# Kernel optimization log

Hardware: AMD Instinct MI355X
Metric: run time of the kernel (lower is better)

## Reference

```python
import jax, jax.numpy as jnp
import numpy as np

LEVELS = np.array([8, 5, 5, 5], dtype=np.int64)
BASIS = np.cumprod(np.concatenate([[1], LEVELS[:-1]])).astype(np.int64)  # [1,8,40,200]
N_E = int(np.prod(LEVELS))  # 1000
BN_EPS = 1e-5
BOUND_EPS = 1e-3


def setup_inputs() -> dict:
    key = jax.random.key(0)
    ks = jax.random.split(key, 3)
    B, C, T, E = 32, 512, 4096, 4
    return {
        "z": jax.random.normal(ks[0], (B, C, T), dtype=jnp.float32),
        "W_in": jax.random.normal(ks[1], (C, E), dtype=jnp.float32) * 0.05,
        "b_in": jnp.zeros((E,), dtype=jnp.float32),
        "gamma": jnp.ones((E,), dtype=jnp.float32),
        "beta": jnp.zeros((E,), dtype=jnp.float32),
        "W_out": jax.random.normal(ks[2], (E, C), dtype=jnp.float32) * 0.05,
        "b_out": jnp.zeros((C,), dtype=jnp.float32),
    }


def _round_ste(x):
    return x + jax.lax.stop_gradient(jnp.round(x) - x)


def reference(z, W_in, b_in, gamma, beta, W_out, b_out):
    levels = jnp.asarray(LEVELS, dtype=jnp.float32)      # [E]
    basis = jnp.asarray(BASIS, dtype=jnp.float32)        # [E]
    half_w = jnp.floor(levels / 2.0)                     # levels // 2
    B, C, T = z.shape
    N = B * T

    # preprocess: 'n c t -> (n t) c'
    x = jnp.transpose(z, (0, 2, 1)).reshape(N, C)        # [N, C]
    # project_in
    h = x @ W_in + b_in                                   # [N, E]
    # BatchNorm1d, training mode (biased batch stats)
    mu = jnp.mean(h, axis=0)
    var = jnp.var(h, axis=0)
    h = (h - mu) * jax.lax.rsqrt(var + BN_EPS) * gamma + beta

    # bound + round_ste quantize
    half_l = (levels - 1.0) * (1.0 - BOUND_EPS) / 2.0
    offset = jnp.where(jnp.mod(levels, 2.0) == 0.0, 0.5, 0.0)
    shift = jnp.tan(offset / half_l)
    bounded = jnp.tanh(h + shift) * half_l - offset
    zhat_n = _round_ste(bounded) / half_w                 # [N, E], normalized codes

    # codes -> indices
    idx = jnp.sum((zhat_n * half_w + half_w) * basis, axis=-1).astype(jnp.int32)  # [N]

    # project_out, '(b t) c -> b c t'
    out = zhat_n @ W_out + b_out                          # [N, C]
    zhat = jnp.transpose(out.reshape(B, T, C), (0, 2, 1))  # [B, C, T]

    commit_loss = jnp.mean((z - jax.lax.stop_gradient(zhat)) ** 2)

    # perplexity via counts (avoids [N, n_e] one-hot)
    counts = jnp.zeros((N_E,), dtype=jnp.float32).at[idx].add(1.0)
    e_mean = counts / N
    perplexity = jnp.exp(-jnp.sum(e_mean * jnp.log(e_mean + 1e-10)))

    return zhat, commit_loss, perplexity
```

## Files before the change

### kernel.cpp

```cpp
#include <hip/hip_runtime.h>
#include <math.h>


namespace {
constexpr int Bv = 32, Cv = 512, Tv = 4096;
constexpr int Nv = Bv * Tv;
constexpr long long TOTv = (long long)Nv * Cv;
constexpr int NTILES = Nv / 256;
constexpr int CSPLIT = 4;
constexpr int CL = Cv / CSPLIT;

constexpr size_t OFF_H   = 0;
constexpr size_t OFF_G   = OFF_H  + (size_t)Nv * 4 * sizeof(double);
constexpr size_t OFF_BS  = OFF_G  + (size_t)Nv * 4 * sizeof(float);
constexpr size_t OFF_CST = OFF_BS + (size_t)NTILES * 10 * sizeof(double);
constexpr size_t OFF_CNT = OFF_CST + 32 * sizeof(double);
constexpr size_t OFF_CP  = OFF_CNT + 4096;
constexpr size_t OFF_WD  = OFF_CP  + (size_t)NTILES * sizeof(double);
constexpr size_t OFF_WT  = OFF_WD  + 2048 * sizeof(double);
}

__global__ void fsq_k0(const float* __restrict__ W_in, const float* __restrict__ W_out,
                       double* __restrict__ winD, float* __restrict__ woutT)
{
    const int i = blockIdx.x * 256 + threadIdx.x;
    if (i < 2048) {
        winD[i] = (double)W_in[i];
        const int c = i >> 2, e = i & 3;
        woutT[i] = W_out[e * 512 + c];
    }
}

__global__ __launch_bounds__(256) void fsq_kA(
    const float* __restrict__ z, const double* __restrict__ winD,
    const float* __restrict__ woutT, const float* __restrict__ b_out,
    const float* __restrict__ b_in,
    double* __restrict__ h_ws, float* __restrict__ g_ws, double* __restrict__ bs_ws)
{
    __shared__ double red[256][10];
    const int tid = threadIdx.x;
    const int blk = blockIdx.x;
    const int b = blk >> 4;
    const int tile = blk & 15;
    const int t = tile * 256 + tid;
    const float* zp = z + (size_t)b * Cv * Tv + t;

    double h0 = 0.0, h1 = 0.0, h2 = 0.0, h3 = 0.0;
    float g0 = 0.f, g1 = 0.f, g2 = 0.f, g3 = 0.f, zbp = 0.f, z2p = 0.f;
#pragma unroll 8
    for (int c = 0; c < Cv; ++c) {
        const float zv = zp[(size_t)c * Tv];
        const double zd = (double)zv;
        h0 = fma(zd, winD[c * 4 + 0], h0);
        h1 = fma(zd, winD[c * 4 + 1], h1);
        h2 = fma(zd, winD[c * 4 + 2], h2);
        h3 = fma(zd, winD[c * 4 + 3], h3);
        g0 = fmaf(zv, woutT[c * 4 + 0], g0);
        g1 = fmaf(zv, woutT[c * 4 + 1], g1);
        g2 = fmaf(zv, woutT[c * 4 + 2], g2);
        g3 = fmaf(zv, woutT[c * 4 + 3], g3);
        zbp = fmaf(zv, b_out[c], zbp);
        z2p = fmaf(zv, zv, z2p);
    }
    h0 += (double)b_in[0]; h1 += (double)b_in[1];
    h2 += (double)b_in[2]; h3 += (double)b_in[3];

    const int n = blk * 256 + tid;
    double* hp = h_ws + (size_t)n * 4;
    double2 hA; hA.x = h0; hA.y = h1;
    double2 hB; hB.x = h2; hB.y = h3;
    *(double2*)(hp)     = hA;
    *(double2*)(hp + 2) = hB;
    *(float4*)(g_ws + (size_t)n * 4) = make_float4(g0, g1, g2, g3);

    red[tid][0] = h0; red[tid][1] = h1; red[tid][2] = h2; red[tid][3] = h3;
    red[tid][4] = h0 * h0; red[tid][5] = h1 * h1; red[tid][6] = h2 * h2; red[tid][7] = h3 * h3;
    red[tid][8] = (double)z2p; red[tid][9] = (double)zbp;
    __syncthreads();
    for (int s = 128; s > 0; s >>= 1) {
        if (tid < s) {
#pragma unroll
            for (int k = 0; k < 10; ++k) red[tid][k] += red[tid + s][k];
        }
        __syncthreads();
    }
    if (tid == 0) {
#pragma unroll
        for (int k = 0; k < 10; ++k) bs_ws[blk * 10 + k] = red[0][k];
    }
}

__global__ __launch_bounds__(512) void fsq_kB(
    const float* __restrict__ gamma, const float* __restrict__ beta,
    const float* __restrict__ W_out, const float* __restrict__ b_out,
    const double* __restrict__ bs_ws, double* __restrict__ consts,
    unsigned* __restrict__ counts)
{
    __shared__ double buf[512 * 15];
    const int tid = threadIdx.x;
#pragma unroll
    for (int k = 0; k < 10; ++k) buf[tid * 15 + k] = bs_ws[tid * 10 + k];
    __syncthreads();
    for (int s = 256; s > 0; s >>= 1) {
        if (tid < s) {
#pragma unroll
            for (int k = 0; k < 10; ++k) buf[tid * 15 + k] += buf[(tid + s) * 15 + k];
        }
        __syncthreads();
    }
    double Sh[4] = {0, 0, 0, 0}, Sq[4] = {0, 0, 0, 0}, SZ2 = 0, SZB = 0;
    if (tid == 0) {
        Sh[0] = buf[0]; Sh[1] = buf[1]; Sh[2] = buf[2]; Sh[3] = buf[3];
        Sq[0] = buf[4]; Sq[1] = buf[5]; Sq[2] = buf[6]; Sq[3] = buf[7];
        SZ2 = buf[8]; SZB = buf[9];
    }
    __syncthreads();
    {
        const int c = tid;
        const double w0 = W_out[c], w1 = W_out[512 + c], w2 = W_out[1024 + c], w3 = W_out[1536 + c];
        const double bb = b_out[c];
        double* r = buf + tid * 15;
        r[0] = w0 * w0; r[1] = w0 * w1; r[2] = w0 * w2; r[3] = w0 * w3;
        r[4] = w1 * w1; r[5] = w1 * w2; r[6] = w1 * w3;
        r[7] = w2 * w2; r[8] = w2 * w3; r[9] = w3 * w3;
        r[10] = w0 * bb; r[11] = w1 * bb; r[12] = w2 * bb; r[13] = w3 * bb; r[14] = bb * bb;
    }
    __syncthreads();
    for (int s = 256; s > 0; s >>= 1) {
        if (tid < s) {
#pragma unroll
            for (int k = 0; k < 15; ++k) buf[tid * 15 + k] += buf[(tid + s) * 15 + k];
        }
        __syncthreads();
    }
    if (tid == 0) {
        const double Ninv = 1.0 / (double)Nv;
#pragma unroll
        for (int e = 0; e < 4; ++e) {
            const double mu = Sh[e] * Ninv;
            const double var = Sq[e] * Ninv - mu * mu;
            const double sc = (double)gamma[e] / sqrt(var + 1e-5);
            consts[e] = sc;
            consts[4 + e] = (double)beta[e] - mu * sc;
        }
        consts[8 + 0]  = buf[0]; consts[8 + 1]  = buf[1]; consts[8 + 2]  = buf[2]; consts[8 + 3]  = buf[3];
        consts[8 + 4]  = buf[1]; consts[8 + 5]  = buf[4]; consts[8 + 6]  = buf[5]; consts[8 + 7]  = buf[6];
        consts[8 + 8]  = buf[2]; consts[8 + 9]  = buf[5]; consts[8 + 10] = buf[7]; consts[8 + 11] = buf[8];
        consts[8 + 12] = buf[3]; consts[8 + 13] = buf[6]; consts[8 + 14] = buf[8]; consts[8 + 15] = buf[9];
        consts[24] = buf[10]; consts[25] = buf[11]; consts[26] = buf[12]; consts[27] = buf[13];
        consts[28] = buf[14];
        consts[29] = SZ2; consts[30] = SZB;
        consts[31] = tan(0.5 / ((8.0 - 1.0) * (1.0 - 1e-3) / 2.0));
    }
    for (int i = tid; i < 1000; i += 512) counts[i] = 0;
}

__global__ __launch_bounds__(256) void fsq_kC(
    const float* __restrict__ woutT, const float* __restrict__ b_out,
    const double* __restrict__ h_ws, const float* __restrict__ g_ws,
    const double* __restrict__ consts, unsigned* __restrict__ counts,
    double* __restrict__ cp_ws, float* __restrict__ out)
{
    __shared__ double red[256];
    const int tid = threadIdx.x;
    const int nt = blockIdx.x;
    const int ys = blockIdx.y;
    const int n = nt * 256 + tid;

    const double sc0 = consts[0], sc1 = consts[1], sc2 = consts[2], sc3 = consts[3];
    const double bi0 = consts[4], bi1 = consts[5], bi2 = consts[6], bi3 = consts[7];
    const double shift0 = consts[31];

    const double* hp = h_ws + (size_t)n * 4;
    const double hn0 = fma(hp[0], sc0, bi0);
    const double hn1 = fma(hp[1], sc1, bi1);
    const double hn2 = fma(hp[2], sc2, bi2);
    const double hn3 = fma(hp[3], sc3, bi3);

    constexpr double hl0 = (8.0 - 1.0) * (1.0 - 1e-3) / 2.0;
    constexpr double hl1 = (5.0 - 1.0) * (1.0 - 1e-3) / 2.0;
    const double r0 = rint(tanh(hn0 + shift0) * hl0 - 0.5);
    const double r1 = rint(tanh(hn1) * hl1);
    const double r2 = rint(tanh(hn2) * hl1);
    const double r3 = rint(tanh(hn3) * hl1);
    const double zd0 = r0 * 0.25, zd1 = r1 * 0.5, zd2 = r2 * 0.5, zd3 = r3 * 0.5;
    const float zn0 = (float)zd0, zn1 = (float)zd1, zn2 = (float)zd2, zn3 = (float)zd3;

    if (ys == 0) {
        const int code = ((int)r0 + 4) + ((int)r1 + 2) * 8 + ((int)r2 + 2) * 40 + ((int)r3 + 2) * 200;
        atomicAdd(&counts[code], 1u);
        const float4 gv = *(const float4*)(g_ws + (size_t)n * 4);
        const double cg = zd0 * (double)gv.x + zd1 * (double)gv.y
                        + zd2 * (double)gv.z + zd3 * (double)gv.w;
        const double znd[4] = {zd0, zd1, zd2, zd3};
        double q = consts[28] + 2.0 * (zd0 * consts[24] + zd1 * consts[25]
                                     + zd2 * consts[26] + zd3 * consts[27]);
#pragma unroll
        for (int e = 0; e < 4; ++e)
#pragma unroll
            for (int f = 0; f < 4; ++f)
                q = fma(znd[e] * znd[f], consts[8 + e * 4 + f], q);
        red[tid] = q - 2.0 * cg;
        __syncthreads();
        for (int s = 128; s > 0; s >>= 1) {
            if (tid < s) red[tid] += red[tid + s];
            __syncthreads();
        }
        if (tid == 0) cp_ws[nt] = red[0];
    }

    const int c0 = ys * CL;
    const size_t base = (size_t)(n >> 12) * ((size_t)Cv * Tv) + (size_t)(n & (Tv - 1));
#pragma unroll 8
    for (int i = 0; i < CL; ++i) {
        const int c = c0 + i;
        float val = b_out[c];
        val = fmaf(zn0, woutT[c * 4 + 0], val);
        val = fmaf(zn1, woutT[c * 4 + 1], val);
        val = fmaf(zn2, woutT[c * 4 + 2], val);
        val = fmaf(zn3, woutT[c * 4 + 3], val);
        out[base + (size_t)c * Tv] = val;
    }
}

__global__ __launch_bounds__(512) void fsq_kD(
    const double* __restrict__ cp_ws, const double* __restrict__ consts,
    const unsigned* __restrict__ counts, float* __restrict__ out, int out_size)
{
    __shared__ double rc[512];
    __shared__ double rp[512];
    const int tid = threadIdx.x;
    double c_ = cp_ws[tid];
    double p_ = 0.0;
    for (int i = tid; i < 1000; i += 512) {
        const double em = (double)counts[i] / (double)Nv;
        p_ += em * log(em + 1e-10);
    }
    rc[tid] = c_; rp[tid] = p_;
    __syncthreads();
    for (int s = 256; s > 0; s >>= 1) {
        if (tid < s) { rc[tid] += rc[tid + s]; rp[tid] += rp[tid + s]; }
        __syncthreads();
    }
    if (tid == 0) {
        const double commit = (consts[29] - 2.0 * consts[30] + rc[0]) / (double)TOTv;
        out[out_size - 2] = (float)commit;
        out[out_size - 1] = (float)exp(-rp[0]);
    }
}

extern "C" void kernel_launch(void* const* d_in, const int* in_sizes, int n_in,
                              void* d_out, int out_size, void* d_ws, size_t ws_size,
                              hipStream_t stream) {
    const float* z     = (const float*)d_in[0];
    const float* W_in  = (const float*)d_in[1];
    const float* b_in  = (const float*)d_in[2];
    const float* gamma = (const float*)d_in[3];
    const float* beta  = (const float*)d_in[4];
    const float* W_out = (const float*)d_in[5];
    const float* b_out = (const float*)d_in[6];
    float* out = (float*)d_out;

    char* ws = (char*)d_ws;
    double*   h_ws   = (double*)(ws + OFF_H);
    float*    g_ws   = (float*)(ws + OFF_G);
    double*   bs_ws  = (double*)(ws + OFF_BS);
    double*   consts = (double*)(ws + OFF_CST);
    unsigned* counts = (unsigned*)(ws + OFF_CNT);
    double*   cp_ws  = (double*)(ws + OFF_CP);
    double*   winD   = (double*)(ws + OFF_WD);
    float*    woutT  = (float*)(ws + OFF_WT);

    fsq_k0<<<8, 256, 0, stream>>>(W_in, W_out, winD, woutT);
    fsq_kA<<<NTILES, 256, 0, stream>>>(z, winD, woutT, b_out, b_in, h_ws, g_ws, bs_ws);
    fsq_kB<<<1, 512, 0, stream>>>(gamma, beta, W_out, b_out, bs_ws, consts, counts);
    fsq_kC<<<dim3(NTILES, CSPLIT), 256, 0, stream>>>(woutT, b_out, h_ws, g_ws, consts,
                                                     counts, cp_ws, out);
    fsq_kD<<<1, 512, 0, stream>>>(cp_ws, consts, counts, out, out_size);
}
```

Before: 177.0 us.

## Restructure FSQ pipeline into channel-split float4 kernels with fp32 accumulation

Replaces the five-kernel pipeline with four kernels. The first kernel splits the channel reduction across four blocks per tile, has each thread handle four timesteps with float4 loads, stages weights in LDS, and accumulates in fp32 instead of fp64. A second kernel combines the partials and computes the per-block BN statistics. A third kernel redundantly reduces the global statistics in every block, which removes the single-block stats kernel, and then writes the output as float4 per channel. The intent is more memory-level parallelism, fewer slow fp64 FMAs and fewer serial launches, at the cost of extra partial-sum traffic and lower precision in the projection that could flip rounding codes.

```diff
diff --git a/kernel.cpp b/kernel.cpp
--- a/kernel.cpp
+++ b/kernel.cpp
@@ -3,249 +3,343 @@
 
 
 namespace {
-constexpr int Bv = 32, Cv = 512, Tv = 4096;
+constexpr int Cv = 512, Tv = 4096, Bv = 32;
 constexpr int Nv = Bv * Tv;
 constexpr long long TOTv = (long long)Nv * Cv;
-constexpr int NTILES = Nv / 256;
-constexpr int CSPLIT = 4;
-constexpr int CL = Cv / CSPLIT;
-
-constexpr size_t OFF_H   = 0;
-constexpr size_t OFF_G   = OFF_H  + (size_t)Nv * 4 * sizeof(double);
-constexpr size_t OFF_BS  = OFF_G  + (size_t)Nv * 4 * sizeof(float);
-constexpr size_t OFF_CST = OFF_BS + (size_t)NTILES * 10 * sizeof(double);
-constexpr size_t OFF_CNT = OFF_CST + 32 * sizeof(double);
-constexpr size_t OFF_CP  = OFF_CNT + 4096;
-constexpr size_t OFF_WD  = OFF_CP  + (size_t)NTILES * sizeof(double);
-constexpr size_t OFF_WT  = OFF_WD  + 2048 * sizeof(double);
-}
-
-__global__ void fsq_k0(const float* __restrict__ W_in, const float* __restrict__ W_out,
-                       double* __restrict__ winD, float* __restrict__ woutT)
+constexpr int CS = 4;
+constexpr int CL = Cv / CS;
+constexpr int NT = 128;
+constexpr int NB = NT * CS;
+
+constexpr size_t OFF_HP  = 0;
+constexpr size_t OFF_GP  = OFF_HP  + (size_t)CS * Nv * 16;
+constexpr size_t OFF_HG  = OFF_GP  + (size_t)CS * Nv * 16;
+constexpr size_t OFF_BS1 = OFF_HG  + (size_t)Nv * 32;
+constexpr size_t OFF_BS2 = OFF_BS1 + (size_t)NB * 2 * 8;
+constexpr size_t OFF_GRM = OFF_BS2 + (size_t)NB * 8 * 8;
+constexpr size_t OFF_CP  = OFF_GRM + 16 * 8;
+constexpr size_t OFF_CNT = OFF_CP  + (size_t)NT * 8;
+}
+
+__global__ __launch_bounds__(256) void fsq_p1(
+    const float* __restrict__ z, const float* __restrict__ W_in,
+    const float* __restrict__ W_out, const float* __restrict__ b_out,
+    float* __restrict__ hpart, float* __restrict__ gpart,
+    double* __restrict__ bs1, double* __restrict__ gram,
+    unsigned* __restrict__ counts)
 {
-    const int i = blockIdx.x * 256 + threadIdx.x;
-    if (i < 2048) {
-        winD[i] = (double)W_in[i];
-        const int c = i >> 2, e = i & 3;
-        woutT[i] = W_out[e * 512 + c];
-    }
-}
-
-__global__ __launch_bounds__(256) void fsq_kA(
-    const float* __restrict__ z, const double* __restrict__ winD,
-    const float* __restrict__ woutT, const float* __restrict__ b_out,
-    const float* __restrict__ b_in,
-    double* __restrict__ h_ws, float* __restrict__ g_ws, double* __restrict__ bs_ws)
+    __shared__ double red[15 * 256];
+    __shared__ float s_wi[CL][4];
+    __shared__ float s_wo[CL][4];
+    __shared__ float s_bo[CL];
+
+    const int tid = threadIdx.x;
+    const int bid = blockIdx.x;
+    const int tile = bid >> 2, cs = bid & 3;
+    const int b = tile >> 2;
+    const int t0 = (tile & 3) * 1024;
+    const int c0 = cs * CL;
+
+    if (bid == 0) {
+        for (int i = tid; i < 1000; i += 256) counts[i] = 0;
+    }
+    if (tid < CL) {
+        const int c = c0 + tid;
+        const float4 wi = *(const float4*)(W_in + c * 4);
+        s_wi[tid][0] = wi.x; s_wi[tid][1] = wi.y; s_wi[tid][2] = wi.z; s_wi[tid][3] = wi.w;
+        s_wo[tid][0] = W_out[c];
+        s_wo[tid][1] = W_out[512 + c];
+        s_wo[tid][2] = W_out[1024 + c];
+        s_wo[tid][3] = W_out[1536 + c];
+        s_bo[tid] = b_out[c];
+    }
+    __syncthreads();
+
+    float h[4][4] = {}, g[4][4] = {};
+    float z2 = 0.f, zb = 0.f;
+    const float* zp = z + ((size_t)b * Cv + c0) * Tv + t0 + tid * 4;
+
+#pragma unroll 4
+    for (int i = 0; i < CL; ++i) {
+        const float4 zv = *(const float4*)(zp + (size_t)i * Tv);
+        const float w0 = s_wi[i][0], w1 = s_wi[i][1], w2 = s_wi[i][2], w3 = s_wi[i][3];
+        const float u0 = s_wo[i][0], u1 = s_wo[i][1], u2 = s_wo[i][2], u3 = s_wo[i][3];
+        const float bo = s_bo[i];
+        const float zr[4] = {zv.x, zv.y, zv.z, zv.w};
+#pragma unroll
+        for (int j = 0; j < 4; ++j) {
+            h[j][0] = fmaf(zr[j], w0, h[j][0]);
+            h[j][1] = fmaf(zr[j], w1, h[j][1]);
+            h[j][2] = fmaf(zr[j], w2, h[j][2]);
+            h[j][3] = fmaf(zr[j], w3, h[j][3]);
+            g[j][0] = fmaf(zr[j], u0, g[j][0]);
+            g[j][1] = fmaf(zr[j], u1, g[j][1]);
+            g[j][2] = fmaf(zr[j], u2, g[j][2]);
+            g[j][3] = fmaf(zr[j], u3, g[j][3]);
+            z2 = fmaf(zr[j], zr[j], z2);
+        }
+        zb = fmaf((zr[0] + zr[1]) + (zr[2] + zr[3]), bo, zb);
+    }
+
+    const size_t n0 = (size_t)tile * 1024 + (size_t)tid * 4;
+    {
+        float* hp = hpart + ((size_t)cs * Nv + n0) * 4;
+        float* gp = gpart + ((size_t)cs * Nv + n0) * 4;
+#pragma unroll
+        for (int j = 0; j < 4; ++j) {
+            *(float4*)(hp + j * 4) = make_float4(h[j][0], h[j][1], h[j][2], h[j][3]);
+            *(float4*)(gp + j * 4) = make_float4(g[j][0], g[j][1], g[j][2], g[j][3]);
+        }
+    }
+
+    red[tid] = (double)z2;
+    red[256 + tid] = (double)zb;
+    __syncthreads();
+    for (int s = 128; s > 0; s >>= 1) {
+        if (tid < s) { red[tid] += red[tid + s]; red[256 + tid] += red[256 + tid + s]; }
+        __syncthreads();
+    }
+    if (tid == 0) { bs1[bid * 2] = red[0]; bs1[bid * 2 + 1] = red[256]; }
+
+    if (bid == NB - 1) {
+        double a[15];
+#pragma unroll
+        for (int k = 0; k < 15; ++k) a[k] = 0.0;
+#pragma unroll
+        for (int r = 0; r < 2; ++r) {
+            const int c = tid + r * 256;
+            const double w0 = (double)W_out[c], w1 = (double)W_out[512 + c];
+            const double w2 = (double)W_out[1024 + c], w3 = (double)W_out[1536 + c];
+            const double bb = (double)b_out[c];
+            a[0] += w0 * w0; a[1] += w0 * w1; a[2] += w0 * w2; a[3] += w0 * w3;
+            a[4] += w1 * w1; a[5] += w1 * w2; a[6] += w1 * w3;
+            a[7] += w2 * w2; a[8] += w2 * w3; a[9] += w3 * w3;
+            a[10] += w0 * bb; a[11] += w1 * bb; a[12] += w2 * bb; a[13] += w3 * bb;
+            a[14] += bb * bb;
+        }
+        __syncthreads();
+#pragma unroll
+        for (int k = 0; k < 15; ++k) red[k * 256 + tid] = a[k];
+        __syncthreads();
+        for (int s = 128; s > 0; s >>= 1) {
+            if (tid < s) {
+#pragma unroll
+                for (int k = 0; k < 15; ++k) red[k * 256 + tid] += red[k * 256 + tid + s];
+            }
+            __syncthreads();
+        }
+        if (tid == 0) {
+#pragma unroll
+            for (int k = 0; k < 15; ++k) gram[k] = red[k * 256];
+        }
+    }
+}
+
+__global__ __launch_bounds__(256) void fsq_p2(
+    const float* __restrict__ hpart, const float* __restrict__ gpart,
+    const float* __restrict__ b_in, float* __restrict__ hg,
+    double* __restrict__ bs2)
 {
-    __shared__ double red[256][10];
+    __shared__ double red[8 * 256];
     const int tid = threadIdx.x;
-    const int blk = blockIdx.x;
-    const int b = blk >> 4;
-    const int tile = blk & 15;
-    const int t = tile * 256 + tid;
-    const float* zp = z + (size_t)b * Cv * Tv + t;
-
-    double h0 = 0.0, h1 = 0.0, h2 = 0.0, h3 = 0.0;
-    float g0 = 0.f, g1 = 0.f, g2 = 0.f, g3 = 0.f, zbp = 0.f, z2p = 0.f;
-#pragma unroll 8
-    for (int c = 0; c < Cv; ++c) {
-        const float zv = zp[(size_t)c * Tv];
-        const double zd = (double)zv;
-        h0 = fma(zd, winD[c * 4 + 0], h0);
-        h1 = fma(zd, winD[c * 4 + 1], h1);
-        h2 = fma(zd, winD[c * 4 + 2], h2);
-        h3 = fma(zd, winD[c * 4 + 3], h3);
-        g0 = fmaf(zv, woutT[c * 4 + 0], g0);
-        g1 = fmaf(zv, woutT[c * 4 + 1], g1);
-        g2 = fmaf(zv, woutT[c * 4 + 2], g2);
-        g3 = fmaf(zv, woutT[c * 4 + 3], g3);
-        zbp = fmaf(zv, b_out[c], zbp);
-        z2p = fmaf(zv, zv, z2p);
-    }
-    h0 += (double)b_in[0]; h1 += (double)b_in[1];
-    h2 += (double)b_in[2]; h3 += (double)b_in[3];
-
-    const int n = blk * 256 + tid;
-    double* hp = h_ws + (size_t)n * 4;
-    double2 hA; hA.x = h0; hA.y = h1;
-    double2 hB; hB.x = h2; hB.y = h3;
-    *(double2*)(hp)     = hA;
-    *(double2*)(hp + 2) = hB;
-    *(float4*)(g_ws + (size_t)n * 4) = make_float4(g0, g1, g2, g3);
-
-    red[tid][0] = h0; red[tid][1] = h1; red[tid][2] = h2; red[tid][3] = h3;
-    red[tid][4] = h0 * h0; red[tid][5] = h1 * h1; red[tid][6] = h2 * h2; red[tid][7] = h3 * h3;
-    red[tid][8] = (double)z2p; red[tid][9] = (double)zbp;
+    const int bid = blockIdx.x;
+    const size_t n = (size_t)bid * 256 + tid;
+
+    const float4 p0 = *(const float4*)(hpart + n * 4);
+    const float4 p1 = *(const float4*)(hpart + ((size_t)Nv + n) * 4);
+    const float4 p2 = *(const float4*)(hpart + ((size_t)2 * Nv + n) * 4);
+    const float4 p3 = *(const float4*)(hpart + ((size_t)3 * Nv + n) * 4);
+    double hd[4];
+    hd[0] = (((double)p0.x + (double)p1.x) + ((double)p2.x + (double)p3.x)) + (double)b_in[0];
+    hd[1] = (((double)p0.y + (double)p1.y) + ((double)p2.y + (double)p3.y)) + (double)b_in[1];
+    hd[2] = (((double)p0.z + (double)p1.z) + ((double)p2.z + (double)p3.z)) + (double)b_in[2];
+    hd[3] = (((double)p0.w + (double)p1.w) + ((double)p2.w + (double)p3.w)) + (double)b_in[3];
+
+    const float4 q0 = *(const float4*)(gpart + n * 4);
+    const float4 q1 = *(const float4*)(gpart + ((size_t)Nv + n) * 4);
+    const float4 q2 = *(const float4*)(gpart + ((size_t)2 * Nv + n) * 4);
+    const float4 q3 = *(const float4*)(gpart + ((size_t)3 * Nv + n) * 4);
+    float gs[4];
+    gs[0] = (q0.x + q1.x) + (q2.x + q3.x);
+    gs[1] = (q0.y + q1.y) + (q2.y + q3.y);
+    gs[2] = (q0.z + q1.z) + (q2.z + q3.z);
+    gs[3] = (q0.w + q1.w) + (q2.w + q3.w);
+
+    *(float4*)(hg + n * 8)     = make_float4((float)hd[0], (float)hd[1], (float)hd[2], (float)hd[3]);
+    *(float4*)(hg + n * 8 + 4) = make_float4(gs[0], gs[1], gs[2], gs[3]);
+
+#pragma unroll
+    for (int e = 0; e < 4; ++e) {
+        red[e * 256 + tid] = hd[e];
+        red[(4 + e) * 256 + tid] = hd[e] * hd[e];
+    }
     __syncthreads();
     for (int s = 128; s > 0; s >>= 1) {
         if (tid < s) {
 #pragma unroll
-            for (int k = 0; k < 10; ++k) red[tid][k] += red[tid + s][k];
+            for (int k = 0; k < 8; ++k) red[k * 256 + tid] += red[k * 256 + tid + s];
         }
         __syncthreads();
     }
     if (tid == 0) {
 #pragma unroll
-        for (int k = 0; k < 10; ++k) bs_ws[blk * 10 + k] = red[0][k];
-    }
-}
-
-__global__ __launch_bounds__(512) void fsq_kB(
-    const float* __restrict__ gamma, const float* __restrict__ beta,
-    const float* __restrict__ W_out, const float* __restrict__ b_out,
-    const double* __restrict__ bs_ws, double* __restrict__ consts,
-    unsigned* __restrict__ counts)
+        for (int k = 0; k < 8; ++k) bs2[bid * 8 + k] = red[k * 256];
+    }
+}
+
+__global__ __launch_bounds__(256) void fsq_p3(
+    const float* __restrict__ hg, const float* __restrict__ W_out,
+    const float* __restrict__ b_out, const float* __restrict__ gamma,
+    const float* __restrict__ beta, const double* __restrict__ bs2,
+    const double* __restrict__ gram, unsigned* __restrict__ counts,
+    double* __restrict__ cp, float* __restrict__ out)
 {
-    __shared__ double buf[512 * 15];
+    __shared__ double red[8 * 256];
+    __shared__ float s_wo[CL][4];
+    __shared__ float s_bo[CL];
+    __shared__ double s_cst[8];
+    __shared__ double s_gr[15];
+
     const int tid = threadIdx.x;
-#pragma unroll
-    for (int k = 0; k < 10; ++k) buf[tid * 15 + k] = bs_ws[tid * 10 + k];
-    __syncthreads();
-    for (int s = 256; s > 0; s >>= 1) {
-        if (tid < s) {
-#pragma unroll
-            for (int k = 0; k < 10; ++k) buf[tid * 15 + k] += buf[(tid + s) * 15 + k];
-        }
-        __syncthreads();
-    }
-    double Sh[4] = {0, 0, 0, 0}, Sq[4] = {0, 0, 0, 0}, SZ2 = 0, SZB = 0;
-    if (tid == 0) {
-        Sh[0] = buf[0]; Sh[1] = buf[1]; Sh[2] = buf[2]; Sh[3] = buf[3];
-        Sq[0] = buf[4]; Sq[1] = buf[5]; Sq[2] = buf[6]; Sq[3] = buf[7];
-        SZ2 = buf[8]; SZB = buf[9];
-    }
-    __syncthreads();
+    const int bid = blockIdx.x;
+    const int tile = bid >> 2, cs = bid & 3;
+    const int b = tile >> 2;
+    const int t0 = (tile & 3) * 1024;
+    const int c0 = cs * CL;
+
+    if (tid < CL) {
+        const int c = c0 + tid;
+        s_wo[tid][0] = W_out[c];
+        s_wo[tid][1] = W_out[512 + c];
+        s_wo[tid][2] = W_out[1024 + c];
+        s_wo[tid][3] = W_out[1536 + c];
+        s_bo[tid] = b_out[c];
+    }
+    if (tid < 15) s_gr[tid] = gram[tid];
+
     {
-        const int c = tid;
-        const double w0 = W_out[c], w1 = W_out[512 + c], w2 = W_out[1024 + c], w3 = W_out[1536 + c];
-        const double bb = b_out[c];
-        double* r = buf + tid * 15;
-        r[0] = w0 * w0; r[1] = w0 * w1; r[2] = w0 * w2; r[3] = w0 * w3;
-        r[4] = w1 * w1; r[5] = w1 * w2; r[6] = w1 * w3;
-        r[7] = w2 * w2; r[8] = w2 * w3; r[9] = w3 * w3;
-        r[10] = w0 * bb; r[11] = w1 * bb; r[12] = w2 * bb; r[13] = w3 * bb; r[14] = bb * bb;
-    }
-    __syncthreads();
-    for (int s = 256; s > 0; s >>= 1) {
-        if (tid < s) {
-#pragma unroll
-            for (int k = 0; k < 15; ++k) buf[tid * 15 + k] += buf[(tid + s) * 15 + k];
-        }
-        __syncthreads();
-    }
-    if (tid == 0) {
-        const double Ninv = 1.0 / (double)Nv;
-#pragma unroll
-        for (int e = 0; e < 4; ++e) {
-            const double mu = Sh[e] * Ninv;
-            const double var = Sq[e] * Ninv - mu * mu;
-            const double sc = (double)gamma[e] / sqrt(var + 1e-5);
-            consts[e] = sc;
-            consts[4 + e] = (double)beta[e] - mu * sc;
-        }
-        consts[8 + 0]  = buf[0]; consts[8 + 1]  = buf[1]; consts[8 + 2]  = buf[2]; consts[8 + 3]  = buf[3];
-        consts[8 + 4]  = buf[1]; consts[8 + 5]  = buf[4]; consts[8 + 6]  = buf[5]; consts[8 + 7]  = buf[6];
-        consts[8 + 8]  = buf[2]; consts[8 + 9]  = buf[5]; consts[8 + 10] = buf[7]; consts[8 + 11] = buf[8];
-        consts[8 + 12] = buf[3]; consts[8 + 13] = buf[6]; consts[8 + 14] = buf[8]; consts[8 + 15] = buf[9];
-        consts[24] = buf[10]; consts[25] = buf[11]; consts[26] = buf[12]; consts[27] = buf[13];
-        consts[28] = buf[14];
-        consts[29] = SZ2; consts[30] = SZB;
-        consts[31] = tan(0.5 / ((8.0 - 1.0) * (1.0 - 1e-3) / 2.0));
-    }
-    for (int i = tid; i < 1000; i += 512) counts[i] = 0;
-}
-
-__global__ __launch_bounds__(256) void fsq_kC(
-    const float* __restrict__ woutT, const float* __restrict__ b_out,
-    const double* __restrict__ h_ws, const float* __restrict__ g_ws,
-    const double* __restrict__ consts, unsigned* __restrict__ counts,
-    double* __restrict__ cp_ws, float* __restrict__ out)
-{
-    __shared__ double red[256];
-    const int tid = threadIdx.x;
-    const int nt = blockIdx.x;
-    const int ys = blockIdx.y;
-    const int n = nt * 256 + tid;
-
-    const double sc0 = consts[0], sc1 = consts[1], sc2 = consts[2], sc3 = consts[3];
-    const double bi0 = consts[4], bi1 = consts[5], bi2 = consts[6], bi3 = consts[7];
-    const double shift0 = consts[31];
-
-    const double* hp = h_ws + (size_t)n * 4;
-    const double hn0 = fma(hp[0], sc0, bi0);
-    const double hn1 = fma(hp[1], sc1, bi1);
-    const double hn2 = fma(hp[2], sc2, bi2);
-    const double hn3 = fma(hp[3], sc3, bi3);
-
+        const double* r0 = bs2 + (size_t)tid * 8;
+        const double* r1 = bs2 + (size_t)(tid + 256) * 8;
+        double a[8];
+#pragma unroll
+        for (int k = 0; k < 8; ++k) a[k] = r0[k] + r1[k];
+#pragma unroll
+        for (int k = 0; k < 8; ++k) red[k * 256 + tid] = a[k];
+        __syncthreads();
+        for (int s = 128; s > 0; s >>= 1) {
+            if (tid < s) {
+#pragma unroll
+                for (int k = 0; k < 8; ++k) red[k * 256 + tid] += red[k * 256 + tid + s];
+            }
+            __syncthreads();
+        }
+        if (tid == 0) {
+            const double Ninv = 1.0 / (double)Nv;
+#pragma unroll
+            for (int e = 0; e < 4; ++e) {
+                const double mu = red[e * 256] * Ninv;
+                const double var = red[(4 + e) * 256] * Ninv - mu * mu;
+                const double sc = (double)gamma[e] / sqrt(var + 1e-5);
+                s_cst[e] = sc;
+                s_cst[4 + e] = (double)beta[e] - mu * sc;
+            }
+        }
+        __syncthreads();
+    }
+
+    const double sc0 = s_cst[0], sc1 = s_cst[1], sc2 = s_cst[2], sc3 = s_cst[3];
+    const double bi0 = s_cst[4], bi1 = s_cst[5], bi2 = s_cst[6], bi3 = s_cst[7];
     constexpr double hl0 = (8.0 - 1.0) * (1.0 - 1e-3) / 2.0;
     constexpr double hl1 = (5.0 - 1.0) * (1.0 - 1e-3) / 2.0;
-    const double r0 = rint(tanh(hn0 + shift0) * hl0 - 0.5);
-    const double r1 = rint(tanh(hn1) * hl1);
-    const double r2 = rint(tanh(hn2) * hl1);
-    const double r3 = rint(tanh(hn3) * hl1);
-    const double zd0 = r0 * 0.25, zd1 = r1 * 0.5, zd2 = r2 * 0.5, zd3 = r3 * 0.5;
-    const float zn0 = (float)zd0, zn1 = (float)zd1, zn2 = (float)zd2, zn3 = (float)zd3;
-
-    if (ys == 0) {
-        const int code = ((int)r0 + 4) + ((int)r1 + 2) * 8 + ((int)r2 + 2) * 40 + ((int)r3 + 2) * 200;
-        atomicAdd(&counts[code], 1u);
-        const float4 gv = *(const float4*)(g_ws + (size_t)n * 4);
-        const double cg = zd0 * (double)gv.x + zd1 * (double)gv.y
-                        + zd2 * (double)gv.z + zd3 * (double)gv.w;
-        const double znd[4] = {zd0, zd1, zd2, zd3};
-        double q = consts[28] + 2.0 * (zd0 * consts[24] + zd1 * consts[25]
-                                     + zd2 * consts[26] + zd3 * consts[27]);
-#pragma unroll
-        for (int e = 0; e < 4; ++e)
-#pragma unroll
-            for (int f = 0; f < 4; ++f)
-                q = fma(znd[e] * znd[f], consts[8 + e * 4 + f], q);
-        red[tid] = q - 2.0 * cg;
+    const double shift0 = tan(0.5 / hl0);
+
+    const size_t n0 = (size_t)tile * 1024 + (size_t)tid * 4;
+    float zn[4][4];
+    double qsum = 0.0;
+#pragma unroll
+    for (int j = 0; j < 4; ++j) {
+        const float4 ha = *(const float4*)(hg + (n0 + j) * 8);
+        const double hn0 = fma((double)ha.x, sc0, bi0);
+        const double hn1 = fma((double)ha.y, sc1, bi1);
+        const double hn2 = fma((double)ha.z, sc2, bi2);
+        const double hn3 = fma((double)ha.w, sc3, bi3);
+        const double r0 = rint(tanh(hn0 + shift0) * hl0 - 0.5);
+        const double r1 = rint(tanh(hn1) * hl1);
+        const double r2 = rint(tanh(hn2) * hl1);
+        const double r3 = rint(tanh(hn3) * hl1);
+        const double zd0 = r0 * 0.25, zd1 = r1 * 0.5, zd2 = r2 * 0.5, zd3 = r3 * 0.5;
+        zn[j][0] = (float)zd0; zn[j][1] = (float)zd1;
+        zn[j][2] = (float)zd2; zn[j][3] = (float)zd3;
+        if (cs == 0) {
+            const float4 ga = *(const float4*)(hg + (n0 + j) * 8 + 4);
+            const int code = ((int)r0 + 4) + ((int)r1 + 2) * 8 + ((int)r2 + 2) * 40
+                           + ((int)r3 + 2) * 200;
+            atomicAdd(&counts[code], 1u);
+            const double cg = zd0 * (double)ga.x + zd1 * (double)ga.y
+                            + zd2 * (double)ga.z + zd3 * (double)ga.w;
+            double q = s_gr[14]
+                     + 2.0 * (zd0 * s_gr[10] + zd1 * s_gr[11] + zd2 * s_gr[12] + zd3 * s_gr[13])
+                     + zd0 * zd0 * s_gr[0] + zd1 * zd1 * s_gr[4]
+                     + zd2 * zd2 * s_gr[7] + zd3 * zd3 * s_gr[9]
+                     + 2.0 * (zd0 * zd1 * s_gr[1] + zd0 * zd2 * s_gr[2] + zd0 * zd3 * s_gr[3]
+                            + zd1 * zd2 * s_gr[5] + zd1 * zd3 * s_gr[6] + zd2 * zd3 * s_gr[8]);
+            qsum += q - 2.0 * cg;
+        }
+    }
+
+    if (cs == 0) {
+        red[tid] = qsum;
         __syncthreads();
         for (int s = 128; s > 0; s >>= 1) {
             if (tid < s) red[tid] += red[tid + s];
             __syncthreads();
         }
-        if (tid == 0) cp_ws[nt] = red[0];
-    }
-
-    const int c0 = ys * CL;
-    const size_t base = (size_t)(n >> 12) * ((size_t)Cv * Tv) + (size_t)(n & (Tv - 1));
-#pragma unroll 8
+        if (tid == 0) cp[tile] = red[0];
+    }
+
+    float* op = out + ((size_t)b * Cv + c0) * Tv + t0 + tid * 4;
+#pragma unroll 4
     for (int i = 0; i < CL; ++i) {
-        const int c = c0 + i;
-        float val = b_out[c];
-        val = fmaf(zn0, woutT[c * 4 + 0], val);
-        val = fmaf(zn1, woutT[c * 4 + 1], val);
-        val = fmaf(zn2, woutT[c * 4 + 2], val);
-        val = fmaf(zn3, woutT[c * 4 + 3], val);
-        out[base + (size_t)c * Tv] = val;
-    }
-}
-
-__global__ __launch_bounds__(512) void fsq_kD(
-    const double* __restrict__ cp_ws, const double* __restrict__ consts,
+        const float u0 = s_wo[i][0], u1 = s_wo[i][1], u2 = s_wo[i][2], u3 = s_wo[i][3];
+        const float bo = s_bo[i];
+        float4 o;
+        o.x = fmaf(zn[0][0], u0, fmaf(zn[0][1], u1, fmaf(zn[0][2], u2, fmaf(zn[0][3], u3, bo))));
+        o.y = fmaf(zn[1][0], u0, fmaf(zn[1][1], u1, fmaf(zn[1][2], u2, fmaf(zn[1][3], u3, bo))));
+        o.z = fmaf(zn[2][0], u0, fmaf(zn[2][1], u1, fmaf(zn[2][2], u2, fmaf(zn[2][3], u3, bo))));
+        o.w = fmaf(zn[3][0], u0, fmaf(zn[3][1], u1, fmaf(zn[3][2], u2, fmaf(zn[3][3], u3, bo))));
+        *(float4*)(op + (size_t)i * Tv) = o;
+    }
+}
+
+__global__ __launch_bounds__(256) void fsq_p4(
+    const double* __restrict__ bs1, const double* __restrict__ cp,
     const unsigned* __restrict__ counts, float* __restrict__ out, int out_size)
 {
-    __shared__ double rc[512];
-    __shared__ double rp[512];
+    __shared__ double red[4 * 256];
     const int tid = threadIdx.x;
-    double c_ = cp_ws[tid];
-    double p_ = 0.0;
-    for (int i = tid; i < 1000; i += 512) {
+    double cv = (tid < NT) ? cp[tid] : 0.0;
+    const double a2 = bs1[tid * 2] + bs1[(tid + 256) * 2];
+    const double ab = bs1[tid * 2 + 1] + bs1[(tid + 256) * 2 + 1];
+    double pl = 0.0;
+    for (int i = tid; i < 1000; i += 256) {
         const double em = (double)counts[i] / (double)Nv;
-        p_ += em * log(em + 1e-10);
-    }
-    rc[tid] = c_; rp[tid] = p_;
+        pl += em * log(em + 1e-10);
+    }
+    red[tid] = cv; red[256 + tid] = a2; red[512 + tid] = ab; red[768 + tid] = pl;
     __syncthreads();
-    for (int s = 256; s > 0; s >>= 1) {
-        if (tid < s) { rc[tid] += rc[tid + s]; rp[tid] += rp[tid + s]; }
+    for (int s = 128; s > 0; s >>= 1) {
+        if (tid < s) {
+            red[tid] += red[tid + s];
+            red[256 + tid] += red[256 + tid + s];
+            red[512 + tid] += red[512 + tid + s];
+            red[768 + tid] += red[768 + tid + s];
+        }
         __syncthreads();
     }
     if (tid == 0) {
-        const double commit = (consts[29] - 2.0 * consts[30] + rc[0]) / (double)TOTv;
+        const double commit = (red[256] - 2.0 * red[512] + red[0]) / (double)TOTv;
         out[out_size - 2] = (float)commit;
-        out[out_size - 1] = (float)exp(-rp[0]);
+        out[out_size - 1] = (float)exp(-red[768]);
     }
 }
 
@@ -262,19 +356,17 @@
     float* out = (float*)d_out;
 
     char* ws = (char*)d_ws;
-    double*   h_ws   = (double*)(ws + OFF_H);
-    float*    g_ws   = (float*)(ws + OFF_G);
-    double*   bs_ws  = (double*)(ws + OFF_BS);
-    double*   consts = (double*)(ws + OFF_CST);
+    float*    hpart  = (float*)(ws + OFF_HP);
+    float*    gpart  = (float*)(ws + OFF_GP);
+    float*    hg     = (float*)(ws + OFF_HG);
+    double*   bs1    = (double*)(ws + OFF_BS1);
+    double*   bs2    = (double*)(ws + OFF_BS2);
+    double*   gram   = (double*)(ws + OFF_GRM);
+    double*   cp     = (double*)(ws + OFF_CP);
     unsigned* counts = (unsigned*)(ws + OFF_CNT);
-    double*   cp_ws  = (double*)(ws + OFF_CP);
-    double*   winD   = (double*)(ws + OFF_WD);
-    float*    woutT  = (float*)(ws + OFF_WT);
-
-    fsq_k0<<<8, 256, 0, stream>>>(W_in, W_out, winD, woutT);
-    fsq_kA<<<NTILES, 256, 0, stream>>>(z, winD, woutT, b_out, b_in, h_ws, g_ws, bs_ws);
-    fsq_kB<<<1, 512, 0, stream>>>(gamma, beta, W_out, b_out, bs_ws, consts, counts);
-    fsq_kC<<<dim3(NTILES, CSPLIT), 256, 0, stream>>>(woutT, b_out, h_ws, g_ws, consts,
-                                                     counts, cp_ws, out);
-    fsq_kD<<<1, 512, 0, stream>>>(cp_ws, consts, counts, out, out_size);
-}
+
+    fsq_p1<<<NB, 256, 0, stream>>>(z, W_in, W_out, b_out, hpart, gpart, bs1, gram, counts);
+    fsq_p2<<<NB, 256, 0, stream>>>(hpart, gpart, b_in, hg, bs2);
+    fsq_p3<<<NB, 256, 0, stream>>>(hg, W_out, b_out, gamma, beta, bs2, gram, counts, cp, out);
+    fsq_p4<<<1, 256, 0, stream>>>(bs1, cp, counts, out, out_size);
+}
```

Result: slower. 198.4 us (+12.1%).
